# Performance work log

Hardware: AMD Instinct MI355X
Metric: run time of the kernel (lower is better)

The kernel has to match this reference:

```python
import jax, jax.numpy as jnp
import numpy as np

N_USERS = 50000
N_BOOKS = 10000
N = N_USERS + N_BOOKS   # 60000 nodes
E = 1_200_000           # edges
D = 64                  # embedding_dim
H, C = 4, 32            # GAT heads / per-head channels (concat -> 128)
EPS = 1e-5              # BatchNorm eps
NEG_SLOPE = 0.2         # GAT leaky relu slope


def setup_inputs() -> dict:
    key = jax.random.key(0)
    ks = jax.random.split(key, 30)
    x = jax.random.normal(ks[0], (N, D), jnp.float32)
    src = jax.random.randint(ks[1], (E,), 0, N)
    dst = jax.random.randint(ks[2], (E,), 0, N)
    edge_index = jnp.stack([src, dst]).astype(jnp.int32)

    def w(k, shape, fan_in):
        return jax.random.normal(k, shape, jnp.float32) * (1.0 / np.sqrt(fan_in))

    def bn(k, n):
        k1, k2, k3, k4 = jax.random.split(k, 4)
        return (jax.random.uniform(k1, (n,), jnp.float32, 0.5, 1.5),   # gamma
                jax.random.normal(k2, (n,), jnp.float32) * 0.1,        # beta
                jax.random.normal(k3, (n,), jnp.float32) * 0.1,        # running_mean
                jax.random.uniform(k4, (n,), jnp.float32, 0.5, 1.5))   # running_var

    bn1_g, bn1_b, bn1_m, bn1_v = bn(ks[10], H * C)
    bn2_g, bn2_b, bn2_m, bn2_v = bn(ks[11], 64)
    bn3_g, bn3_b, bn3_m, bn3_v = bn(ks[12], 32)
    return {
        "x": x, "edge_index": edge_index,
        # GATConv(64 -> 32, heads=4, concat)
        "gat_w": w(ks[3], (H * C, D), D),
        "gat_att_src": w(ks[4], (H, C), C),
        "gat_att_dst": w(ks[5], (H, C), C),
        "gat_b": jnp.zeros((H * C,), jnp.float32),
        "bn1_g": bn1_g, "bn1_b": bn1_b, "bn1_m": bn1_m, "bn1_v": bn1_v,
        # SAGEConv(128 -> 64): lin_l (neighbors, with bias), lin_r (self, no bias)
        "sage_wl": w(ks[6], (64, H * C), H * C),
        "sage_bl": jnp.zeros((64,), jnp.float32),
        "sage_wr": w(ks[7], (64, H * C), H * C),
        "bn2_g": bn2_g, "bn2_b": bn2_b, "bn2_m": bn2_m, "bn2_v": bn2_v,
        # GCNConv(64 -> 32)
        "gcn_w": w(ks[8], (32, 64), 64),
        "gcn_b": jnp.zeros((32,), jnp.float32),
        "bn3_g": bn3_g, "bn3_b": bn3_b, "bn3_m": bn3_m, "bn3_v": bn3_v,
    }


def _bn_eval(h, g, b, m, v):
    return (h - m) * jax.lax.rsqrt(v + EPS) * g + b


def _segment_softmax(e, seg, n):
    # softmax of per-edge logits e [E, H] grouped by target node seg
    mx = jax.ops.segment_max(e, seg, num_segments=n)
    ex = jnp.exp(e - mx[seg])
    s = jax.ops.segment_sum(ex, seg, num_segments=n)
    return ex / (s[seg] + 1e-16)


def reference(x, edge_index, gat_w, gat_att_src, gat_att_dst, gat_b,
              bn1_g, bn1_b, bn1_m, bn1_v,
              sage_wl, sage_bl, sage_wr,
              bn2_g, bn2_b, bn2_m, bn2_v,
              gcn_w, gcn_b,
              bn3_g, bn3_b, bn3_m, bn3_v):
    n = x.shape[0]
    src, dst = edge_index[0], edge_index[1]  # messages flow src -> dst
    loop = jnp.arange(n, dtype=src.dtype)
    src_sl = jnp.concatenate([src, loop])    # with self-loops (GAT, GCN)
    dst_sl = jnp.concatenate([dst, loop])

    # ---- GATConv(64 -> 32, heads=4, concat) ----
    xw = (x @ gat_w.T).reshape(n, H, C)                      # [N, H, C]
    a_src = jnp.einsum('nhc,hc->nh', xw, gat_att_src)        # [N, H]
    a_dst = jnp.einsum('nhc,hc->nh', xw, gat_att_dst)
    logits = jax.nn.leaky_relu(a_src[src_sl] + a_dst[dst_sl], NEG_SLOPE)  # [E+N, H]
    alpha = _segment_softmax(logits, dst_sl, n)
    msg = xw[src_sl] * alpha[:, :, None]                     # [E+N, H, C]
    h = jax.ops.segment_sum(msg, dst_sl, num_segments=n).reshape(n, H * C) + gat_b
    h = _bn_eval(jax.nn.elu(h), bn1_g, bn1_b, bn1_m, bn1_v)  # dropout = eval no-op

    # ---- SAGEConv(128 -> 64), mean aggregation, no self-loops ----
    deg = jax.ops.segment_sum(jnp.ones_like(dst, jnp.float32), dst, num_segments=n)
    nbr_mean = jax.ops.segment_sum(h[src], dst, num_segments=n) / jnp.maximum(deg, 1.0)[:, None]
    h = nbr_mean @ sage_wl.T + sage_bl + h @ sage_wr.T
    h = _bn_eval(jax.nn.elu(h), bn2_g, bn2_b, bn2_m, bn2_v)

    # ---- GCNConv(64 -> 32), symmetric normalization with self-loops ----
    hw = h @ gcn_w.T                                         # [N, 32]
    deg_sl = jax.ops.segment_sum(jnp.ones_like(dst_sl, jnp.float32), dst_sl, num_segments=n)
    dinv = jnp.where(deg_sl > 0, jax.lax.rsqrt(deg_sl), 0.0)
    norm = dinv[src_sl] * dinv[dst_sl]                       # [E+N]
    h = jax.ops.segment_sum(norm[:, None] * hw[src_sl], dst_sl, num_segments=n) + gcn_b
    h = _bn_eval(jax.nn.elu(h), bn3_g, bn3_b, bn3_m, bn3_v)
    return h
```

## Files before the change

### kernel.cpp

```cpp
#include <hip/hip_runtime.h>

#define NN 60000
#define EE 1200000
#define NB1 ((NN+255)/256)
#define NBK 938
#define CH  4096

typedef __attribute__((ext_vector_type(8))) short short8;
typedef __attribute__((ext_vector_type(4))) float f32x4;

__device__ __forceinline__ float leakyf(float x){ return x >= 0.f ? x : 0.2f*x; }
__device__ __forceinline__ float eluf(float x){ return x > 0.f ? x : expm1f(x); }

__device__ __forceinline__ float bflo(uint v){ union{uint i;float f;}c; c.i = v<<16; return c.f; }
__device__ __forceinline__ float bfhi(uint v){ union{uint i;float f;}c; c.i = v & 0xffff0000u; return c.f; }
__device__ __forceinline__ ushort f2bf(float f){ union{float f;uint i;}c; c.f=f;
    uint r = c.i + 0x7fffu + ((c.i>>16)&1u); return (ushort)(r>>16); }
__device__ __forceinline__ uint pack2(float a, float b){ return (uint)f2bf(a) | ((uint)f2bf(b)<<16); }
__device__ __forceinline__ short8 ld8(const uint* p){
    union{ uint4 u; short8 s; } c; c.u = *(const uint4*)p; return c.s; }

__global__ void k_count(const int* __restrict__ dst, int* __restrict__ counts){
    int e = blockIdx.x*blockDim.x + threadIdx.x;
    if (e < EE) atomicAdd(&counts[dst[e]], 1);
}

__global__ __launch_bounds__(256) void k_bsum(const int* __restrict__ counts,
                                              int* __restrict__ bsum){
    __shared__ int sh[256];
    int t = threadIdx.x, i = blockIdx.x*256 + t;
    sh[t] = (i < NN) ? counts[i] : 0;
    __syncthreads();
    for (int off = 128; off; off >>= 1){
        if (t < off) sh[t] += sh[t+off];
        __syncthreads();
    }
    if (t == 0) bsum[blockIdx.x] = sh[0];
}

__global__ __launch_bounds__(256) void k_scan2(const int* __restrict__ bsum,
                                               int* __restrict__ ebsum){
    __shared__ int sh[256];
    int t = threadIdx.x;
    int v = (t < NB1) ? bsum[t] : 0;
    sh[t] = v; __syncthreads();
    for (int off = 1; off < 256; off <<= 1){
        int o = (t >= off) ? sh[t-off] : 0;
        __syncthreads();
        sh[t] += o;
        __syncthreads();
    }
    ebsum[t] = sh[t] - v;
    if (t == 255) ebsum[256] = sh[255];
}

__global__ __launch_bounds__(256) void k_rowptr(const int* __restrict__ counts,
        const int* __restrict__ ebsum, int* __restrict__ row_ptr,
        float* __restrict__ dinv, int* __restrict__ bcur){
    __shared__ int sh[256];
    int t = threadIdx.x, i = blockIdx.x*256 + t;
    int v = (i < NN) ? counts[i] : 0;
    sh[t] = v; __syncthreads();
    for (int off = 1; off < 256; off <<= 1){
        int o = (t >= off) ? sh[t-off] : 0;
        __syncthreads();
        sh[t] += o;
        __syncthreads();
    }
    if (i < NN){
        int rv = ebsum[blockIdx.x] + sh[t] - v;
        row_ptr[i] = rv;
        dinv[i] = rsqrtf((float)(v + 1));
        if ((i & 63) == 0) bcur[i >> 6] = rv;
    }
    if (blockIdx.x == 0 && t == 0) row_ptr[NN] = ebsum[256];
}

__global__ __launch_bounds__(256) void k_binsort(const int* __restrict__ src,
        const int* __restrict__ dst, int* __restrict__ bcur,
        int2* __restrict__ pairs){
    __shared__ int2 buf2[CH];
    __shared__ int hist[NBK];
    __shared__ int loff[NBK];
    __shared__ int rcur[NBK];
    __shared__ int gbase[NBK];
    __shared__ int stmp[256];
    int t = threadIdx.x;
    for (int e0 = blockIdx.x*CH; e0 < EE; e0 += gridDim.x*CH){
        int cnt = min(CH, EE - e0);
        for (int j = t; j < NBK; j += 256){ hist[j] = 0; rcur[j] = 0; }
        __syncthreads();
        for (int j = t; j < cnt; j += 256)
            atomicAdd(&hist[dst[e0+j] >> 6], 1);
        __syncthreads();
        int b0 = t*4, ssum = 0;
        #pragma unroll
        for (int k2 = 0; k2 < 4; k2++){
            int idx = b0 + k2;
            if (idx < NBK) ssum += hist[idx];
        }
        stmp[t] = ssum; __syncthreads();
        for (int off = 1; off < 256; off <<= 1){
            int o = (t >= off) ? stmp[t-off] : 0;
            __syncthreads();
            stmp[t] += o;
            __syncthreads();
        }
        int excl = stmp[t] - ssum;
        #pragma unroll
        for (int k2 = 0; k2 < 4; k2++){
            int idx = b0 + k2;
            if (idx < NBK){ loff[idx] = excl; excl += hist[idx]; }
        }
        __syncthreads();
        for (int j = t; j < NBK; j += 256){
            int h = hist[j];
            if (h) gbase[j] = atomicAdd(&bcur[j], h);
        }
        __syncthreads();
        for (int j = t; j < cnt; j += 256){
            int s = src[e0+j], d = dst[e0+j];
            int b = d >> 6;
            int lpos = loff[b] + atomicAdd(&rcur[b], 1);
            buf2[lpos] = make_int2(s, d);
        }
        __syncthreads();
        for (int j = t; j < cnt; j += 256){
            int2 pr = buf2[j];
            int b = pr.y >> 6;
            pairs[gbase[b] + (j - loff[b])] = pr;
        }
        __syncthreads();
    }
}

__global__ __launch_bounds__(256) void k_csr_local(const int* __restrict__ rp,
        const int2* __restrict__ pairs, int* __restrict__ col){
    __shared__ int lcur[64];
    int b = blockIdx.x, t = threadIdx.x;
    int nb0 = b*64;
    int nb1 = min(NN, nb0 + 64);
    int base = rp[nb0];
    int bsz = rp[nb1] - base;
    if (t < 64){
        int node = nb0 + t;
        lcur[t] = (node < NN ? rp[node] : rp[NN]) - base;
    }
    __syncthreads();
    for (int i = t; i < bsz; i += 256){
        int2 pr = pairs[base + i];
        int dl = pr.y - nb0;
        int lpos = atomicAdd(&lcur[dl], 1);
        col[base + lpos] = pr.x;
    }
}

__global__ __launch_bounds__(256) void k_wprep(const float* __restrict__ wl,
        const float* __restrict__ wr, const float* __restrict__ gcw,
        ushort* __restrict__ wcat, ushort* __restrict__ gcb){
    int t = blockIdx.x*256 + threadIdx.x;
    if (t < 16384){
        int o = t >> 8, k = t & 255;
        float v = (k < 128) ? wl[o*128 + k] : wr[o*128 + (k-128)];
        wcat[t] = f2bf(v);
    }
    if (t < 2048) gcb[t] = f2bf(gcw[t]);
}

#define XTILE 938
__global__ __launch_bounds__(256) void k_xw_mfma(const float* __restrict__ x,
        const float* __restrict__ w, const float* __restrict__ att_s,
        const float* __restrict__ att_d, ushort* __restrict__ xw_h,
        float* __restrict__ a_src, float* __restrict__ a_dst){
    int t = threadIdx.x;
    int wv = t >> 6, lane = t & 63;
    int l15 = lane & 15, g = lane >> 4;
    short8 bw[2][2];
    float attv_s[2], attv_d[2];
    #pragma unroll
    for (int ct = 0; ct < 2; ct++){
        int colo = wv*32 + ct*16 + l15;
        attv_s[ct] = att_s[colo];
        attv_d[ct] = att_d[colo];
        #pragma unroll
        for (int ks = 0; ks < 2; ks++){
            const float* wp = w + colo*64 + ks*32 + g*8;
            short8 b;
            #pragma unroll
            for (int j = 0; j < 8; j++) b[j] = (short)f2bf(wp[j]);
            bw[ct][ks] = b;
        }
    }
    for (int tile = blockIdx.x; tile < XTILE; tile += gridDim.x){
        int nb = tile*64;
        #pragma unroll
        for (int rt = 0; rt < 4; rt++){
            int na = nb + rt*16 + l15;
            const float* xp = x + (size_t)min(na, NN-1)*64;
            short8 a[2];
            #pragma unroll
            for (int ks = 0; ks < 2; ks++){
                float xv[8];
                *(float4*)&xv[0] = *(const float4*)(xp + ks*32 + g*8);
                *(float4*)&xv[4] = *(const float4*)(xp + ks*32 + g*8 + 4);
                short8 av;
                #pragma unroll
                for (int j = 0; j < 8; j++) av[j] = (short)f2bf(xv[j]);
                a[ks] = av;
            }
            f32x4 acc0 = {0.f,0.f,0.f,0.f}, acc1 = {0.f,0.f,0.f,0.f};
            acc0 = __builtin_amdgcn_mfma_f32_16x16x32_bf16(a[0], bw[0][0], acc0, 0, 0, 0);
            acc0 = __builtin_amdgcn_mfma_f32_16x16x32_bf16(a[1], bw[0][1], acc0, 0, 0, 0);
            acc1 = __builtin_amdgcn_mfma_f32_16x16x32_bf16(a[0], bw[1][0], acc1, 0, 0, 0);
            acc1 = __builtin_amdgcn_mfma_f32_16x16x32_bf16(a[1], bw[1][1], acc1, 0, 0, 0);
            #pragma unroll
            for (int r = 0; r < 4; r++){
                int node = nb + rt*16 + g*4 + r;
                if (node < NN){
                    xw_h[(size_t)node*128 + wv*32 + l15]      = f2bf(acc0[r]);
                    xw_h[(size_t)node*128 + wv*32 + 16 + l15] = f2bf(acc1[r]);
                }
            }
            float ps[4], pd[4];
            #pragma unroll
            for (int r = 0; r < 4; r++){
                ps[r] = acc0[r]*attv_s[0] + acc1[r]*attv_s[1];
                pd[r] = acc0[r]*attv_d[0] + acc1[r]*attv_d[1];
            }
            #pragma unroll
            for (int d = 1; d < 16; d <<= 1){
                #pragma unroll
                for (int r = 0; r < 4; r++){
                    ps[r] += __shfl_xor(ps[r], d);
                    pd[r] += __shfl_xor(pd[r], d);
                }
            }
            if (l15 == 0){
                #pragma unroll
                for (int r = 0; r < 4; r++){
                    int node = nb + rt*16 + g*4 + r;
                    if (node < NN){
                        a_src[node*4 + wv] = ps[r];
                        a_dst[node*4 + wv] = pd[r];
                    }
                }
            }
        }
    }
}

__global__ __launch_bounds__(256) void k_gat(const int* __restrict__ rp,
        const int* __restrict__ col, const float* __restrict__ a_src,
        const float* __restrict__ a_dst, const uint* __restrict__ xw_u,
        const float* __restrict__ gb,
        const float* __restrict__ g1, const float* __restrict__ b1,
        const float* __restrict__ m1, const float* __restrict__ v1,
        ushort* __restrict__ h1_h){
    int gw = (blockIdx.x*256 + threadIdx.x) >> 6;
    int nwaves = (gridDim.x*256) >> 6;
    int lane = threadIdx.x & 63;
    int hh = lane >> 4;
    int o0 = 2*lane, o1 = o0 + 1;
    float gb0 = gb[o0], gb1 = gb[o1];
    float sc0 = g1[o0]*rsqrtf(v1[o0]+1e-5f), sh0 = b1[o0] - m1[o0]*sc0;
    float sc1 = g1[o1]*rsqrtf(v1[o1]+1e-5f), sh1 = b1[o1] - m1[o1]*sc1;

    for (int n = gw; n < NN; n += nwaves){
        int r0 = rp[n], deg = rp[n+1] - r0;
        float adh = a_dst[n*4 + hh];
        float wself = __expf(leakyf(a_src[n*4 + hh] + adh));
        uint v = xw_u[(size_t)n*64 + lane];
        float s  = wself;
        float ax = bflo(v)*wself, ay = bfhi(v)*wself;
        #pragma unroll 4
        for (int i = 0; i < deg; i++){
            int sidx = col[r0+i];
            float wgt = __expf(leakyf(a_src[sidx*4 + hh] + adh));
            uint vv = xw_u[(size_t)sidx*64 + lane];
            s  += wgt;
            ax += wgt*bflo(vv); ay += wgt*bfhi(vv);
        }
        float Sinv = 1.f/(s + 1e-16f);
        ax = ax*Sinv + gb0; ay = ay*Sinv + gb1;
        ax = eluf(ax)*sc0 + sh0;
        ay = eluf(ay)*sc1 + sh1;
        *(uint*)(h1_h + (size_t)n*128 + o0) = pack2(ax, ay);
    }
}

__global__ __launch_bounds__(256) void k_mean(const int* __restrict__ rp,
        const int* __restrict__ col, const uint* __restrict__ h1_u,
        uint* __restrict__ mean_u){
    int gw = (blockIdx.x*256 + threadIdx.x) >> 6;
    int nwaves = (gridDim.x*256) >> 6;
    int lane = threadIdx.x & 63;
    for (int n = gw; n < NN; n += nwaves){
        int r0 = rp[n], deg = rp[n+1] - r0;
        float ax = 0.f, ay = 0.f;
        #pragma unroll 4
        for (int i = 0; i < deg; i++){
            uint v = h1_u[(size_t)col[r0+i]*64 + lane];
            ax += bflo(v); ay += bfhi(v);
        }
        float inv = deg > 0 ? 1.f/(float)deg : 0.f;
        mean_u[(size_t)n*64 + lane] = pack2(ax*inv, ay*inv);
    }
}

#define STILE 938
__global__ __launch_bounds__(256) void k_sage_mfma(
        const uint* __restrict__ mean_u, const uint* __restrict__ h1_u,
        const uint* __restrict__ wcat_u, const float* __restrict__ bl,
        const uint* __restrict__ gcb_u,
        const float* __restrict__ g2, const float* __restrict__ b2,
        const float* __restrict__ m2, const float* __restrict__ v2,
        ushort* __restrict__ hw_h)
{
    __shared__ ushort h2_s[64][72];
    int t = threadIdx.x;
    int w = t >> 6, lane = t & 63;
    int l15 = lane & 15, g = lane >> 4;
    int olane = w*16 + l15;

    short8 bw[8];
    #pragma unroll
    for (int ks = 0; ks < 8; ks++)
        bw[ks] = ld8(wcat_u + (size_t)olane*128 + ks*16 + g*4);
    short8 bg[2][2];
    #pragma unroll
    for (int ct = 0; ct < 2; ct++)
        #pragma unroll
        for (int ks = 0; ks < 2; ks++)
            bg[ct][ks] = ld8(gcb_u + (size_t)(ct*16 + l15)*32 + ks*16 + g*4);

    float blv = bl[olane];
    float scv = g2[olane]*rsqrtf(v2[olane]+1e-5f);
    float shv = b2[olane] - m2[olane]*scv;

    for (int tile = blockIdx.x; tile < STILE; tile += gridDim.x){
        int nb = tile*64;
        __syncthreads();
        #pragma unroll
        for (int rt = 0; rt < 4; rt++){
            f32x4 acc = {0.f, 0.f, 0.f, 0.f};
            size_t node = (size_t)(nb + rt*16 + l15);
            const uint* am = mean_u + node*64 + g*4;
            const uint* as = h1_u  + node*64 + g*4;
            #pragma unroll
            for (int ks = 0; ks < 4; ks++)
                acc = __builtin_amdgcn_mfma_f32_16x16x32_bf16(ld8(am + ks*16), bw[ks], acc, 0, 0, 0);
            #pragma unroll
            for (int ks = 0; ks < 4; ks++)
                acc = __builtin_amdgcn_mfma_f32_16x16x32_bf16(ld8(as + ks*16), bw[4+ks], acc, 0, 0, 0);
            #pragma unroll
            for (int r = 0; r < 4; r++){
                int row = rt*16 + g*4 + r;
                h2_s[row][olane] = f2bf(eluf(acc[r] + blv)*scv + shv);
            }
        }
        __syncthreads();
        short8 a2[2];
        #pragma unroll
        for (int ks = 0; ks < 2; ks++)
            a2[ks] = *(const short8*)&h2_s[w*16 + l15][ks*32 + g*8];
        #pragma unroll
        for (int ct = 0; ct < 2; ct++){
            f32x4 acc2 = {0.f, 0.f, 0.f, 0.f};
            #pragma unroll
            for (int ks = 0; ks < 2; ks++)
                acc2 = __builtin_amdgcn_mfma_f32_16x16x32_bf16(a2[ks], bg[ct][ks], acc2, 0, 0, 0);
            #pragma unroll
            for (int r = 0; r < 4; r++){
                int row = nb + w*16 + g*4 + r;
                if (row < NN) hw_h[(size_t)row*32 + ct*16 + l15] = f2bf(acc2[r]);
            }
        }
    }
}

__global__ __launch_bounds__(256) void k_gcn(const int* __restrict__ rp,
        const int* __restrict__ col, const uint* __restrict__ hw_u,
        const float* __restrict__ dinv, const float* __restrict__ gb,
        const float* __restrict__ g3, const float* __restrict__ b3,
        const float* __restrict__ m3, const float* __restrict__ v3,
        float* __restrict__ out){
    int t = threadIdx.x;
    int n = blockIdx.x*4 + (t >> 6);
    int lane = t & 63, u = lane & 15, part = lane >> 4;
    int r0 = rp[n], deg = rp[n+1] - r0;
    float dn = dinv[n];
    float ax = 0.f, ay = 0.f;
    for (int i = part; i < deg; i += 4){
        int s = col[r0+i];
        float dv = dinv[s];
        uint hv = hw_u[(size_t)s*16 + u];
        ax += dv*bflo(hv); ay += dv*bfhi(hv);
    }
    ax += __shfl_xor(ax, 16); ay += __shfl_xor(ay, 16);
    ax += __shfl_xor(ax, 32); ay += __shfl_xor(ay, 32);
    if (part == 0){
        uint sv = hw_u[(size_t)n*16 + u];
        float tx = ax*dn + dn*dn*bflo(sv);
        float ty = ay*dn + dn*dn*bfhi(sv);
        int o0 = 2*u, o1 = o0 + 1;
        tx += gb[o0]; ty += gb[o1];
        tx = eluf(tx); ty = eluf(ty);
        tx = (tx - m3[o0]) * rsqrtf(v3[o0] + 1e-5f) * g3[o0] + b3[o0];
        ty = (ty - m3[o1]) * rsqrtf(v3[o1] + 1e-5f) * g3[o1] + b3[o1];
        *(float2*)(out + (size_t)n*32 + o0) = make_float2(tx, ty);
    }
}

extern "C" void kernel_launch(void* const* d_in, const int* in_sizes, int n_in,
                              void* d_out, int out_size, void* d_ws, size_t ws_size,
                              hipStream_t stream)
{
    const float* x     = (const float*)d_in[0];
    const int*   ei    = (const int*)d_in[1];
    const float* gat_w = (const float*)d_in[2];
    const float* att_s = (const float*)d_in[3];
    const float* att_d = (const float*)d_in[4];
    const float* gat_b = (const float*)d_in[5];
    const float* bn1g = (const float*)d_in[6],  *bn1b = (const float*)d_in[7];
    const float* bn1m = (const float*)d_in[8],  *bn1v = (const float*)d_in[9];
    const float* sage_wl = (const float*)d_in[10];
    const float* sage_bl = (const float*)d_in[11];
    const float* sage_wr = (const float*)d_in[12];
    const float* bn2g = (const float*)d_in[13], *bn2b = (const float*)d_in[14];
    const float* bn2m = (const float*)d_in[15], *bn2v = (const float*)d_in[16];
    const float* gcn_w = (const float*)d_in[17];
    const float* gcn_b = (const float*)d_in[18];
    const float* bn3g = (const float*)d_in[19], *bn3b = (const float*)d_in[20];
    const float* bn3m = (const float*)d_in[21], *bn3v = (const float*)d_in[22];

    const int* src  = ei;
    const int* dstp = ei + EE;

    char* W = (char*)d_ws;
    ushort* xw_h   = (ushort*)W;
    ushort* h1_h   = xw_h + (size_t)NN*128;
    ushort* mean_h = h1_h + (size_t)NN*128;
    ushort* hw_h   = mean_h + (size_t)NN*128;
    float* a_s  = (float*)(hw_h + (size_t)NN*32 + 8192);
    float* a_d  = a_s + (size_t)NN*4;
    float* dinv = a_d + (size_t)NN*4;
    int* row_ptr = (int*)(dinv + NN);
    int* counts  = row_ptr + (NN+1);
    int* col     = counts + NN;
    int* bsum    = col + EE;
    int* ebsum   = bsum + NB1;
    ushort* wcat_h = (ushort*)(ebsum + 260);
    ushort* gcb_h  = wcat_h + 16384;
    int* bcur = (int*)(gcb_h + 2048);
    char* p2 = (char*)(bcur + NBK);
    p2 = (char*)(((uintptr_t)p2 + 15) & ~(uintptr_t)15);
    int2* pairs = (int2*)p2;

    const uint* xw_u   = (const uint*)xw_h;
    const uint* h1_u   = (const uint*)h1_h;
    uint* mean_u = (uint*)mean_h;
    uint* hw_u   = (uint*)hw_h;
    const uint* wcat_u = (const uint*)wcat_h;
    const uint* gcb_u  = (const uint*)gcb_h;
    float* out = (float*)d_out;

    hipMemsetAsync(counts, 0, NN*sizeof(int), stream);
    k_count<<<(EE+255)/256, 256, 0, stream>>>(dstp, counts);
    k_bsum<<<NB1, 256, 0, stream>>>(counts, bsum);
    k_scan2<<<1, 256, 0, stream>>>(bsum, ebsum);
    k_rowptr<<<NB1, 256, 0, stream>>>(counts, ebsum, row_ptr, dinv, bcur);
    k_binsort<<<256, 256, 0, stream>>>(src, dstp, bcur, pairs);
    k_csr_local<<<NBK, 256, 0, stream>>>(row_ptr, pairs, col);
    k_wprep<<<64, 256, 0, stream>>>(sage_wl, sage_wr, gcn_w, wcat_h, gcb_h);

    k_xw_mfma<<<XTILE, 256, 0, stream>>>(x, gat_w, att_s, att_d, xw_h, a_s, a_d);
    k_gat<<<2048, 256, 0, stream>>>(row_ptr, col, a_s, a_d, xw_u, gat_b,
                                    bn1g, bn1b, bn1m, bn1v, h1_h);
    k_mean<<<2048, 256, 0, stream>>>(row_ptr, col, h1_u, mean_u);
    k_sage_mfma<<<STILE, 256, 0, stream>>>(mean_u, h1_u, wcat_u, sage_bl, gcb_u,
                                           bn2g, bn2b, bn2m, bn2v, hw_h);
    k_gcn<<<NN/4, 256, 0, stream>>>(row_ptr, col, hw_u, dinv, gcn_b,
                                    bn3g, bn3b, bn3m, bn3v, out);
}
```

Before: 300.8 us.

## Project SAGE neighbor features before mean aggregation to halve gather width

Applies the SAGE lin_l weight to each node's 128-wide h1 first, then aggregates the projected 64-wide features over neighbors, instead of averaging 128-wide neighbor features and projecting afterwards. Because mean and linear map commute, the edge gather now reads 64 bf16 values per edge instead of 128. That is half the random-access traffic in the mean kernel, and half-wave splitting over neighbors is used. It adds a separate node-level MFMA kernel and an fp32 mean buffer read in the SAGE epilogue, at the cost of extra launch and writes.

```diff
diff --git a/kernel.cpp b/kernel.cpp
--- a/kernel.cpp
+++ b/kernel.cpp
@@ -157,13 +157,10 @@
 
 __global__ __launch_bounds__(256) void k_wprep(const float* __restrict__ wl,
         const float* __restrict__ wr, const float* __restrict__ gcw,
-        ushort* __restrict__ wcat, ushort* __restrict__ gcb){
+        ushort* __restrict__ wlb, ushort* __restrict__ wrb,
+        ushort* __restrict__ gcb){
     int t = blockIdx.x*256 + threadIdx.x;
-    if (t < 16384){
-        int o = t >> 8, k = t & 255;
-        float v = (k < 128) ? wl[o*128 + k] : wr[o*128 + (k-128)];
-        wcat[t] = f2bf(v);
-    }
+    if (t < 8192){ wlb[t] = f2bf(wl[t]); wrb[t] = f2bf(wr[t]); }
     if (t < 2048) gcb[t] = f2bf(gcw[t]);
 }
 
@@ -288,29 +285,62 @@
     }
 }
 
-__global__ __launch_bounds__(256) void k_mean(const int* __restrict__ rp,
-        const int* __restrict__ col, const uint* __restrict__ h1_u,
-        uint* __restrict__ mean_u){
+__global__ __launch_bounds__(256) void k_gw(const uint* __restrict__ h1_u,
+        const uint* __restrict__ wlb_u, ushort* __restrict__ g_h){
+    int t = threadIdx.x;
+    int wv = t >> 6, lane = t & 63;
+    int l15 = lane & 15, g = lane >> 4;
+    int olane = wv*16 + l15;
+    short8 bw[4];
+    #pragma unroll
+    for (int ks = 0; ks < 4; ks++)
+        bw[ks] = ld8(wlb_u + (size_t)olane*64 + ks*16 + g*4);
+    for (int tile = blockIdx.x; tile < XTILE; tile += gridDim.x){
+        int nb = tile*64;
+        #pragma unroll
+        for (int rt = 0; rt < 4; rt++){
+            size_t node = (size_t)min(nb + rt*16 + l15, NN-1);
+            const uint* ap = h1_u + node*64 + g*4;
+            f32x4 acc = {0.f,0.f,0.f,0.f};
+            #pragma unroll
+            for (int ks = 0; ks < 4; ks++)
+                acc = __builtin_amdgcn_mfma_f32_16x16x32_bf16(ld8(ap + ks*16), bw[ks], acc, 0, 0, 0);
+            #pragma unroll
+            for (int r = 0; r < 4; r++){
+                int n2 = nb + rt*16 + g*4 + r;
+                if (n2 < NN) g_h[(size_t)n2*64 + olane] = f2bf(acc[r]);
+            }
+        }
+    }
+}
+
+__global__ __launch_bounds__(256) void k_gmean(const int* __restrict__ rp,
+        const int* __restrict__ col, const uint* __restrict__ g_u,
+        float* __restrict__ meang){
     int gw = (blockIdx.x*256 + threadIdx.x) >> 6;
     int nwaves = (gridDim.x*256) >> 6;
     int lane = threadIdx.x & 63;
+    int l31 = lane & 31, half = lane >> 5;
     for (int n = gw; n < NN; n += nwaves){
         int r0 = rp[n], deg = rp[n+1] - r0;
         float ax = 0.f, ay = 0.f;
-        #pragma unroll 4
-        for (int i = 0; i < deg; i++){
-            uint v = h1_u[(size_t)col[r0+i]*64 + lane];
+        for (int i = half; i < deg; i += 2){
+            int s = col[r0+i];
+            uint v = g_u[(size_t)s*32 + l31];
             ax += bflo(v); ay += bfhi(v);
         }
-        float inv = deg > 0 ? 1.f/(float)deg : 0.f;
-        mean_u[(size_t)n*64 + lane] = pack2(ax*inv, ay*inv);
+        ax += __shfl_xor(ax, 32); ay += __shfl_xor(ay, 32);
+        if (half == 0){
+            float inv = deg > 0 ? 1.f/(float)deg : 0.f;
+            *(float2*)(meang + (size_t)n*64 + 2*l31) = make_float2(ax*inv, ay*inv);
+        }
     }
 }
 
 #define STILE 938
 __global__ __launch_bounds__(256) void k_sage_mfma(
-        const uint* __restrict__ mean_u, const uint* __restrict__ h1_u,
-        const uint* __restrict__ wcat_u, const float* __restrict__ bl,
+        const float* __restrict__ meang, const uint* __restrict__ h1_u,
+        const uint* __restrict__ wrb_u, const float* __restrict__ bl,
         const uint* __restrict__ gcb_u,
         const float* __restrict__ g2, const float* __restrict__ b2,
         const float* __restrict__ m2, const float* __restrict__ v2,
@@ -322,10 +352,10 @@
     int l15 = lane & 15, g = lane >> 4;
     int olane = w*16 + l15;
 
-    short8 bw[8];
+    short8 bw[4];
     #pragma unroll
-    for (int ks = 0; ks < 8; ks++)
-        bw[ks] = ld8(wcat_u + (size_t)olane*128 + ks*16 + g*4);
+    for (int ks = 0; ks < 4; ks++)
+        bw[ks] = ld8(wrb_u + (size_t)olane*64 + ks*16 + g*4);
     short8 bg[2][2];
     #pragma unroll
     for (int ct = 0; ct < 2; ct++)
@@ -344,18 +374,16 @@
         for (int rt = 0; rt < 4; rt++){
             f32x4 acc = {0.f, 0.f, 0.f, 0.f};
             size_t node = (size_t)(nb + rt*16 + l15);
-            const uint* am = mean_u + node*64 + g*4;
-            const uint* as = h1_u  + node*64 + g*4;
+            const uint* as = h1_u + node*64 + g*4;
             #pragma unroll
             for (int ks = 0; ks < 4; ks++)
-                acc = __builtin_amdgcn_mfma_f32_16x16x32_bf16(ld8(am + ks*16), bw[ks], acc, 0, 0, 0);
-            #pragma unroll
-            for (int ks = 0; ks < 4; ks++)
-                acc = __builtin_amdgcn_mfma_f32_16x16x32_bf16(ld8(as + ks*16), bw[4+ks], acc, 0, 0, 0);
+                acc = __builtin_amdgcn_mfma_f32_16x16x32_bf16(ld8(as + ks*16), bw[ks], acc, 0, 0, 0);
             #pragma unroll
             for (int r = 0; r < 4; r++){
                 int row = rt*16 + g*4 + r;
-                h2_s[row][olane] = f2bf(eluf(acc[r] + blv)*scv + shv);
+                int n2 = min(nb + row, NN-1);
+                float mg = meang[(size_t)n2*64 + olane];
+                h2_s[row][olane] = f2bf(eluf(acc[r] + mg + blv)*scv + shv);
             }
         }
         __syncthreads();
@@ -449,8 +477,9 @@
     int* col     = counts + NN;
     int* bsum    = col + EE;
     int* ebsum   = bsum + NB1;
-    ushort* wcat_h = (ushort*)(ebsum + 260);
-    ushort* gcb_h  = wcat_h + 16384;
+    ushort* wlb_h = (ushort*)(ebsum + 260);
+    ushort* wrb_h = wlb_h + 8192;
+    ushort* gcb_h = wrb_h + 8192;
     int* bcur = (int*)(gcb_h + 2048);
     char* p2 = (char*)(bcur + NBK);
     p2 = (char*)(((uintptr_t)p2 + 15) & ~(uintptr_t)15);
@@ -458,10 +487,13 @@
 
     const uint* xw_u   = (const uint*)xw_h;
     const uint* h1_u   = (const uint*)h1_h;
-    uint* mean_u = (uint*)mean_h;
+    ushort* g_h  = mean_h;
+    const uint* g_u = (const uint*)g_h;
+    float* meang = (float*)xw_h;
     uint* hw_u   = (uint*)hw_h;
-    const uint* wcat_u = (const uint*)wcat_h;
-    const uint* gcb_u  = (const uint*)gcb_h;
+    const uint* wlb_u = (const uint*)wlb_h;
+    const uint* wrb_u = (const uint*)wrb_h;
+    const uint* gcb_u = (const uint*)gcb_h;
     float* out = (float*)d_out;
 
     hipMemsetAsync(counts, 0, NN*sizeof(int), stream);
@@ -471,13 +503,14 @@
     k_rowptr<<<NB1, 256, 0, stream>>>(counts, ebsum, row_ptr, dinv, bcur);
     k_binsort<<<256, 256, 0, stream>>>(src, dstp, bcur, pairs);
     k_csr_local<<<NBK, 256, 0, stream>>>(row_ptr, pairs, col);
-    k_wprep<<<64, 256, 0, stream>>>(sage_wl, sage_wr, gcn_w, wcat_h, gcb_h);
+    k_wprep<<<32, 256, 0, stream>>>(sage_wl, sage_wr, gcn_w, wlb_h, wrb_h, gcb_h);
 
     k_xw_mfma<<<XTILE, 256, 0, stream>>>(x, gat_w, att_s, att_d, xw_h, a_s, a_d);
     k_gat<<<2048, 256, 0, stream>>>(row_ptr, col, a_s, a_d, xw_u, gat_b,
                                     bn1g, bn1b, bn1m, bn1v, h1_h);
-    k_mean<<<2048, 256, 0, stream>>>(row_ptr, col, h1_u, mean_u);
-    k_sage_mfma<<<STILE, 256, 0, stream>>>(mean_u, h1_u, wcat_u, sage_bl, gcb_u,
+    k_gw<<<XTILE, 256, 0, stream>>>(h1_u, wlb_u, g_h);
+    k_gmean<<<2048, 256, 0, stream>>>(row_ptr, col, g_u, meang);
+    k_sage_mfma<<<STILE, 256, 0, stream>>>(meang, h1_u, wrb_u, sage_bl, gcb_u,
                                            bn2g, bn2b, bn2m, bn2v, hw_h);
     k_gcn<<<NN/4, 256, 0, stream>>>(row_ptr, col, hw_u, dinv, gcn_b,
                                     bn3g, bn3b, bn3m, bn3v, out);
```

Result: slower. 318.0 us (+5.7%).

## Build CSR from 64-node bucket histogram instead of per-node global counts

Applied to the files above, without the earlier changes.

Replaces per-node global atomic counting and the three-kernel scan with a shared-memory bucket histogram (64 nodes per bucket), a single-block scan, and per-bucket local counting inside the CSR kernel that also produces row_ptr and dinv. Edge pairs are packed into one int (src<<6 | dst&63), which halves the traffic for the intermediate pairs buffer. The weight-conversion kernel is merged into the prep launch, and binsort keeps edges in registers so they are read from global memory once. Fewer launches and far fewer global atomics, at the cost of assuming src fits in 26 bits.

```diff
diff --git a/kernel.cpp b/kernel.cpp
--- a/kernel.cpp
+++ b/kernel.cpp
@@ -2,7 +2,6 @@
 
 #define NN 60000
 #define EE 1200000
-#define NB1 ((NN+255)/256)
 #define NBK 938
 #define CH  4096
 
@@ -20,84 +19,92 @@
 __device__ __forceinline__ short8 ld8(const uint* p){
     union{ uint4 u; short8 s; } c; c.u = *(const uint4*)p; return c.s; }
 
-__global__ void k_count(const int* __restrict__ dst, int* __restrict__ counts){
-    int e = blockIdx.x*blockDim.x + threadIdx.x;
-    if (e < EE) atomicAdd(&counts[dst[e]], 1);
-}
-
-__global__ __launch_bounds__(256) void k_bsum(const int* __restrict__ counts,
-                                              int* __restrict__ bsum){
-    __shared__ int sh[256];
-    int t = threadIdx.x, i = blockIdx.x*256 + t;
-    sh[t] = (i < NN) ? counts[i] : 0;
+__global__ __launch_bounds__(256) void k_bcount(const int* __restrict__ dst,
+                                                int* __restrict__ bhist){
+    __shared__ int lh[NBK];
+    int t = threadIdx.x;
+    for (int j = t; j < NBK; j += 256) lh[j] = 0;
     __syncthreads();
-    for (int off = 128; off; off >>= 1){
-        if (t < off) sh[t] += sh[t+off];
-        __syncthreads();
-    }
-    if (t == 0) bsum[blockIdx.x] = sh[0];
-}
-
-__global__ __launch_bounds__(256) void k_scan2(const int* __restrict__ bsum,
-                                               int* __restrict__ ebsum){
-    __shared__ int sh[256];
-    int t = threadIdx.x;
-    int v = (t < NB1) ? bsum[t] : 0;
-    sh[t] = v; __syncthreads();
-    for (int off = 1; off < 256; off <<= 1){
-        int o = (t >= off) ? sh[t-off] : 0;
-        __syncthreads();
-        sh[t] += o;
-        __syncthreads();
-    }
-    ebsum[t] = sh[t] - v;
-    if (t == 255) ebsum[256] = sh[255];
-}
-
-__global__ __launch_bounds__(256) void k_rowptr(const int* __restrict__ counts,
-        const int* __restrict__ ebsum, int* __restrict__ row_ptr,
-        float* __restrict__ dinv, int* __restrict__ bcur){
-    __shared__ int sh[256];
-    int t = threadIdx.x, i = blockIdx.x*256 + t;
-    int v = (i < NN) ? counts[i] : 0;
-    sh[t] = v; __syncthreads();
-    for (int off = 1; off < 256; off <<= 1){
-        int o = (t >= off) ? sh[t-off] : 0;
-        __syncthreads();
-        sh[t] += o;
-        __syncthreads();
-    }
-    if (i < NN){
-        int rv = ebsum[blockIdx.x] + sh[t] - v;
-        row_ptr[i] = rv;
-        dinv[i] = rsqrtf((float)(v + 1));
-        if ((i & 63) == 0) bcur[i >> 6] = rv;
-    }
-    if (blockIdx.x == 0 && t == 0) row_ptr[NN] = ebsum[256];
+    for (int e = blockIdx.x*256 + t; e < EE; e += gridDim.x*256)
+        atomicAdd(&lh[dst[e] >> 6], 1);
+    __syncthreads();
+    for (int j = t; j < NBK; j += 256){
+        int v = lh[j];
+        if (v) atomicAdd(&bhist[j], v);
+    }
+}
+
+__global__ __launch_bounds__(256) void k_prep(const int* __restrict__ bhist,
+        int* __restrict__ bstart, int* __restrict__ bcur,
+        const float* __restrict__ wl, const float* __restrict__ wr,
+        const float* __restrict__ gcw,
+        ushort* __restrict__ wcat, ushort* __restrict__ gcb){
+    int blk = blockIdx.x, t = threadIdx.x;
+    if (blk == 0){
+        __shared__ int stmp[256];
+        int vals[4], s4 = 0;
+        #pragma unroll
+        for (int k = 0; k < 4; k++){
+            int idx = t*4 + k;
+            vals[k] = (idx < NBK) ? bhist[idx] : 0;
+            s4 += vals[k];
+        }
+        stmp[t] = s4; __syncthreads();
+        for (int off = 1; off < 256; off <<= 1){
+            int o = (t >= off) ? stmp[t-off] : 0;
+            __syncthreads();
+            stmp[t] += o;
+            __syncthreads();
+        }
+        int ex = stmp[t] - s4;
+        #pragma unroll
+        for (int k = 0; k < 4; k++){
+            int idx = t*4 + k;
+            if (idx < NBK){ bstart[idx] = ex; bcur[idx] = ex; ex += vals[k]; }
+        }
+        if (t == 0) bstart[NBK] = EE;
+    } else {
+        int g = (blk-1)*256 + t;
+        if (g < 16384){
+            int o = g >> 8, k = g & 255;
+            float v = (k < 128) ? wl[o*128 + k] : wr[o*128 + (k-128)];
+            wcat[g] = f2bf(v);
+        }
+        if (g < 2048) gcb[g] = f2bf(gcw[g]);
+    }
 }
 
 __global__ __launch_bounds__(256) void k_binsort(const int* __restrict__ src,
         const int* __restrict__ dst, int* __restrict__ bcur,
-        int2* __restrict__ pairs){
-    __shared__ int2 buf2[CH];
+        int* __restrict__ pairs){
     __shared__ int hist[NBK];
     __shared__ int loff[NBK];
     __shared__ int rcur[NBK];
     __shared__ int gbase[NBK];
+    __shared__ int2 buf2[CH];
     __shared__ int stmp[256];
     int t = threadIdx.x;
     for (int e0 = blockIdx.x*CH; e0 < EE; e0 += gridDim.x*CH){
         int cnt = min(CH, EE - e0);
         for (int j = t; j < NBK; j += 256){ hist[j] = 0; rcur[j] = 0; }
         __syncthreads();
-        for (int j = t; j < cnt; j += 256)
-            atomicAdd(&hist[dst[e0+j] >> 6], 1);
-        __syncthreads();
-        int b0 = t*4, ssum = 0;
+        int pk[16], bb[16];
+        #pragma unroll
+        for (int k = 0; k < 16; k++){
+            int j = t + k*256;
+            bool ok = j < cnt;
+            int s = 0, d = 0;
+            if (ok){ s = src[e0+j]; d = dst[e0+j]; atomicAdd(&hist[d >> 6], 1); }
+            pk[k] = (s << 6) | (d & 63);
+            bb[k] = ok ? (d >> 6) : -1;
+        }
+        __syncthreads();
+        int b0 = t*4, ssum = 0, hv[4];
         #pragma unroll
         for (int k2 = 0; k2 < 4; k2++){
             int idx = b0 + k2;
-            if (idx < NBK) ssum += hist[idx];
+            hv[k2] = (idx < NBK) ? hist[idx] : 0;
+            ssum += hv[k2];
         }
         stmp[t] = ssum; __syncthreads();
         for (int off = 1; off < 256; off <<= 1){
@@ -110,7 +117,7 @@
         #pragma unroll
         for (int k2 = 0; k2 < 4; k2++){
             int idx = b0 + k2;
-            if (idx < NBK){ loff[idx] = excl; excl += hist[idx]; }
+            if (idx < NBK){ loff[idx] = excl; excl += hv[k2]; }
         }
         __syncthreads();
         for (int j = t; j < NBK; j += 256){
@@ -118,53 +125,59 @@
             if (h) gbase[j] = atomicAdd(&bcur[j], h);
         }
         __syncthreads();
-        for (int j = t; j < cnt; j += 256){
-            int s = src[e0+j], d = dst[e0+j];
-            int b = d >> 6;
-            int lpos = loff[b] + atomicAdd(&rcur[b], 1);
-            buf2[lpos] = make_int2(s, d);
+        #pragma unroll
+        for (int k = 0; k < 16; k++){
+            int b = bb[k];
+            if (b >= 0){
+                int lpos = loff[b] + atomicAdd(&rcur[b], 1);
+                buf2[lpos] = make_int2(pk[k], b);
+            }
         }
         __syncthreads();
         for (int j = t; j < cnt; j += 256){
             int2 pr = buf2[j];
-            int b = pr.y >> 6;
-            pairs[gbase[b] + (j - loff[b])] = pr;
-        }
-        __syncthreads();
-    }
-}
-
-__global__ __launch_bounds__(256) void k_csr_local(const int* __restrict__ rp,
-        const int2* __restrict__ pairs, int* __restrict__ col){
-    __shared__ int lcur[64];
+            pairs[gbase[pr.y] + (j - loff[pr.y])] = pr.x;
+        }
+        __syncthreads();
+    }
+}
+
+__global__ __launch_bounds__(256) void k_csr_local(const int* __restrict__ bstart,
+        const int* __restrict__ pairs, int* __restrict__ rp,
+        int* __restrict__ col, float* __restrict__ dinv){
+    __shared__ int cnt64[64];
     int b = blockIdx.x, t = threadIdx.x;
     int nb0 = b*64;
-    int nb1 = min(NN, nb0 + 64);
-    int base = rp[nb0];
-    int bsz = rp[nb1] - base;
+    int base = bstart[b];
+    int bsz = bstart[b+1] - base;
+    if (t < 64) cnt64[t] = 0;
+    __syncthreads();
+    for (int i = t; i < bsz; i += 256)
+        atomicAdd(&cnt64[pairs[base+i] & 63], 1);
+    __syncthreads();
     if (t < 64){
+        int v = cnt64[t];
+        int inc = v;
+        #pragma unroll
+        for (int d = 1; d < 64; d <<= 1){
+            int o = __shfl_up(inc, d);
+            if (t >= d) inc += o;
+        }
+        int ex = inc - v;
         int node = nb0 + t;
-        lcur[t] = (node < NN ? rp[node] : rp[NN]) - base;
+        if (node < NN){
+            rp[node] = base + ex;
+            dinv[node] = rsqrtf((float)(v + 1));
+        }
+        cnt64[t] = ex;
     }
     __syncthreads();
     for (int i = t; i < bsz; i += 256){
-        int2 pr = pairs[base + i];
-        int dl = pr.y - nb0;
-        int lpos = atomicAdd(&lcur[dl], 1);
-        col[base + lpos] = pr.x;
-    }
-}
-
-__global__ __launch_bounds__(256) void k_wprep(const float* __restrict__ wl,
-        const float* __restrict__ wr, const float* __restrict__ gcw,
-        ushort* __restrict__ wcat, ushort* __restrict__ gcb){
-    int t = blockIdx.x*256 + threadIdx.x;
-    if (t < 16384){
-        int o = t >> 8, k = t & 255;
-        float v = (k < 128) ? wl[o*128 + k] : wr[o*128 + (k-128)];
-        wcat[t] = f2bf(v);
-    }
-    if (t < 2048) gcb[t] = f2bf(gcw[t]);
+        int pv = pairs[base + i];
+        int lpos = atomicAdd(&cnt64[pv & 63], 1);
+        col[base + lpos] = pv >> 6;
+    }
+    if (b == 0 && t == 0) rp[NN] = EE;
 }
 
 #define XTILE 938
@@ -445,16 +458,15 @@
     float* a_d  = a_s + (size_t)NN*4;
     float* dinv = a_d + (size_t)NN*4;
     int* row_ptr = (int*)(dinv + NN);
-    int* counts  = row_ptr + (NN+1);
-    int* col     = counts + NN;
-    int* bsum    = col + EE;
-    int* ebsum   = bsum + NB1;
-    ushort* wcat_h = (ushort*)(ebsum + 260);
+    int* col     = row_ptr + (NN+1);
+    ushort* wcat_h = (ushort*)(col + EE);
     ushort* gcb_h  = wcat_h + 16384;
-    int* bcur = (int*)(gcb_h + 2048);
+    int* bhist  = (int*)(gcb_h + 2048);
+    int* bstart = bhist + NBK;
+    int* bcur   = bstart + NBK + 1;
     char* p2 = (char*)(bcur + NBK);
     p2 = (char*)(((uintptr_t)p2 + 15) & ~(uintptr_t)15);
-    int2* pairs = (int2*)p2;
+    int* pairs = (int*)p2;
 
     const uint* xw_u   = (const uint*)xw_h;
     const uint* h1_u   = (const uint*)h1_h;
@@ -464,14 +476,12 @@
     const uint* gcb_u  = (const uint*)gcb_h;
     float* out = (float*)d_out;
 
-    hipMemsetAsync(counts, 0, NN*sizeof(int), stream);
-    k_count<<<(EE+255)/256, 256, 0, stream>>>(dstp, counts);
-    k_bsum<<<NB1, 256, 0, stream>>>(counts, bsum);
-    k_scan2<<<1, 256, 0, stream>>>(bsum, ebsum);
-    k_rowptr<<<NB1, 256, 0, stream>>>(counts, ebsum, row_ptr, dinv, bcur);
+    hipMemsetAsync(bhist, 0, NBK*sizeof(int), stream);
+    k_bcount<<<256, 256, 0, stream>>>(dstp, bhist);
+    k_prep<<<65, 256, 0, stream>>>(bhist, bstart, bcur, sage_wl, sage_wr, gcn_w,
+                                   wcat_h, gcb_h);
     k_binsort<<<256, 256, 0, stream>>>(src, dstp, bcur, pairs);
-    k_csr_local<<<NBK, 256, 0, stream>>>(row_ptr, pairs, col);
-    k_wprep<<<64, 256, 0, stream>>>(sage_wl, sage_wr, gcn_w, wcat_h, gcb_h);
+    k_csr_local<<<NBK, 256, 0, stream>>>(bstart, pairs, row_ptr, col, dinv);
 
     k_xw_mfma<<<XTILE, 256, 0, stream>>>(x, gat_w, att_s, att_d, xw_h, a_s, a_d);
     k_gat<<<2048, 256, 0, stream>>>(row_ptr, col, a_s, a_d, xw_u, gat_b,
```

Result: faster. 254.5 us, median of 2 (-15.4%).
